# Performance work log

Hardware: AMD Instinct MI355X
Metric: run time of the kernel (lower is better)

The kernel has to match this reference:

```python
import jax, jax.numpy as jnp
import numpy as np

N_PHOTONS = 20_000_000
HEX_R = 24  # axial hex grid radius -> 3R^2+3R+1 = 1801 pixels
SQRT3 = 3.0 ** 0.5


def _build_sensor():
    # Build pointy-top hex pixel centers on an axial grid (replicates hex_centers input),
    # then replicate HexagonalSensor.__init__ lookup-table construction in numpy.
    size = 1.0
    qs, rs = [], []
    for q in range(-HEX_R, HEX_R + 1):
        for r in range(max(-HEX_R, -q - HEX_R), min(HEX_R, -q + HEX_R) + 1):
            qs.append(q); rs.append(r)
    q = np.array(qs, dtype=np.float64); r = np.array(rs, dtype=np.float64)
    centers = np.stack([size * SQRT3 * (q + r / 2.0), size * 1.5 * r], axis=-1)
    n_pixels = centers.shape[0]
    diff = centers[:, None, :] - centers[None, :, :]
    d = np.sqrt((diff ** 2).sum(-1))
    np.fill_diagonal(d, np.inf)
    hex_size = float(d.min() / SQRT3)
    cx, cy = centers[:, 0], centers[:, 1]
    qa = (SQRT3 / 3.0 * cx - cy / 3.0) / hex_size
    ra = (2.0 / 3.0) * cy / hex_size
    q_offset = float(qa[0] - np.round(qa[0]))
    r_offset = float(ra[0] - np.round(ra[0]))
    q_grid = np.round(qa - q_offset).astype(np.int32)
    r_grid = np.round(ra - r_offset).astype(np.int32)
    q_min = int(q_grid.min()); r_min = int(r_grid.min())
    lookup = np.full((int(q_grid.max()) - q_min + 1, int(r_grid.max()) - r_min + 1), -1, dtype=np.int32)
    lookup[q_grid - q_min, r_grid - r_min] = np.arange(n_pixels)
    return hex_size, q_offset, r_offset, q_min, r_min, n_pixels, jnp.asarray(lookup)


def setup_inputs() -> dict:
    key = jax.random.key(0)
    kx, ky, kv = jax.random.split(key, 3)
    hex_size, q_off, r_off, q_min, r_min, n_pixels, lookup = _build_sensor()
    extent = 45.0  # camera footprint (~sqrt(3)*R + margin) so some photons miss (tests masking)
    x = jax.random.uniform(kx, (N_PHOTONS,), minval=-extent, maxval=extent, dtype=jnp.float32)
    y = jax.random.uniform(ky, (N_PHOTONS,), minval=-extent, maxval=extent, dtype=jnp.float32)
    values = jax.random.uniform(kv, (N_PHOTONS,), dtype=jnp.float32)
    return {"x": x, "y": y, "values": values, "lookup_table": lookup,
            "hex_size": hex_size, "q_offset": q_off, "r_offset": r_off,
            "q_min": q_min, "r_min": r_min, "n_pixels": n_pixels}


def _axial_round(q, r):
    s = -q - r
    qr, rr, sr = jnp.round(q), jnp.round(r), jnp.round(s)
    qd, rd, sd = jnp.abs(qr - q), jnp.abs(rr - r), jnp.abs(sr - s)
    qr2 = jnp.where((qd > rd) & (qd > sd), -rr - sr, qr)
    rr2 = jnp.where((rd > qd) & (rd > sd), -qr - sr, rr)
    return qr2, rr2


def reference(x, y, values, lookup_table, hex_size, q_offset, r_offset, q_min, r_min, n_pixels):
    # Cartesian -> axial hex coords
    q = (SQRT3 / 3.0 * x - y / 3.0) / hex_size
    r = (2.0 / 3.0) * y / hex_size
    qg, rg = _axial_round(q - q_offset, r - r_offset)
    q_idx = qg.astype(jnp.int32) - q_min
    r_idx = rg.astype(jnp.int32) - r_min
    Q, R = lookup_table.shape
    in_bounds = (q_idx >= 0) & (q_idx < Q) & (r_idx >= 0) & (r_idx < R)
    pixel_idx = lookup_table[q_idx.clip(0, Q - 1), r_idx.clip(0, R - 1)]
    valid = in_bounds & (pixel_idx >= 0)
    pixel_idx = jnp.where(valid, pixel_idx, 0)
    vals = jnp.where(valid, values, jnp.zeros((), values.dtype))
    return jax.ops.segment_sum(vals, pixel_idx, num_segments=n_pixels)
```

## Files before the change

### kernel.cpp

```cpp
#include <hip/hip_runtime.h>
#include <math.h>


#define FLUSH_P 64

typedef float f32x4 __attribute__((ext_vector_type(4)));

__global__ void hex_zero_kernel(float* __restrict__ p, int n) {
    int i = blockIdx.x * blockDim.x + threadIdx.x;
    if (i < n) p[i] = 0.0f;
}

__global__ __launch_bounds__(256) void hex_reduce_kernel(
    const float* __restrict__ partials, float* __restrict__ out, int n_pixels)
{
    int pix = blockIdx.x * blockDim.x + threadIdx.x;
    if (pix >= n_pixels) return;
    float s = 0.0f;
    #pragma unroll 8
    for (int j = 0; j < FLUSH_P; ++j) s += partials[j * n_pixels + pix];
    out[pix] = s;
}

__global__ __launch_bounds__(256) void hex_bin_kernel(
    const float* __restrict__ x,
    const float* __restrict__ y,
    const float* __restrict__ vals,
    const float* __restrict__ hex_size_p,
    const float* __restrict__ q_off_p,
    const float* __restrict__ r_off_p,
    const int*   __restrict__ q_min_p,
    const int*   __restrict__ r_min_p,
    int Rh,
    int n_pixels, int n_photons,
    float* __restrict__ flush_dst,
    int use_partials)
{
    extern __shared__ float hist[];
    for (int i = threadIdx.x; i < n_pixels; i += blockDim.x) hist[i] = 0.0f;
    __syncthreads();

    const float inv_h = 1.0f / hex_size_p[0];
    const float A  = 0.57735026918962576f * inv_h;
    const float Bn = -(0.33333333333333333f * inv_h);
    const float C  = 0.66666666666666667f * inv_h;
    const float qc = -q_off_p[0];
    const float rc = -r_off_p[0];
    const int   qmin = q_min_p[0];
    const int   rmin = r_min_p[0];

    const unsigned twoR = (unsigned)(2 * Rh);
    const int Rp1 = Rh + 1;

    auto process = [&](float xf, float yf, float vf) {
        float q = fmaf(A, xf, fmaf(Bn, yf, qc));
        float r = fmaf(C, yf, rc);
        float t = q + r;
        float qr = rintf(q);
        float rr = rintf(r);
        float tr = rintf(t);
        float qd = fabsf(qr - q);
        float rd = fabsf(rr - r);
        float td = fabsf(tr - t);
        float q2 = (qd > rd && qd > td) ? (tr - rr) : qr;
        float r2 = (rd > qd && rd > td) ? (tr - qr) : rr;
        int qi = (int)q2 - qmin;
        int ri = (int)r2 - rmin;
        int d  = qi + ri;
        if ((unsigned)qi <= twoR && (unsigned)ri <= twoR &&
            (unsigned)(d - Rh) <= twoR) {
            int u  = max(qi - Rh, 0);
            int p  = qi * Rp1 + ((qi * qi - qi) >> 1) + d - Rh - u * u;
            atomicAdd(&hist[p], vf);
        }
    };

    const int tid    = blockIdx.x * blockDim.x + threadIdx.x;
    const int stride = gridDim.x * blockDim.x;
    const int n8     = n_photons >> 3;

    const f32x4* __restrict__ x4 = (const f32x4*)x;
    const f32x4* __restrict__ y4 = (const f32x4*)y;
    const f32x4* __restrict__ v4 = (const f32x4*)vals;

    f32x4 xa, xb, ya, yb, va, vb;
    int i = tid;
    if (i < n8) {
        int a = 2 * i, b = a + 1;
        xa = __builtin_nontemporal_load(&x4[a]);
        xb = __builtin_nontemporal_load(&x4[b]);
        ya = __builtin_nontemporal_load(&y4[a]);
        yb = __builtin_nontemporal_load(&y4[b]);
        va = __builtin_nontemporal_load(&v4[a]);
        vb = __builtin_nontemporal_load(&v4[b]);
    }
    while (i < n8) {
        int nx = i + stride;
        f32x4 nxa, nxb, nya, nyb, nva, nvb;
        bool has_next = nx < n8;
        if (has_next) {
            int a = 2 * nx, b = a + 1;
            nxa = __builtin_nontemporal_load(&x4[a]);
            nxb = __builtin_nontemporal_load(&x4[b]);
            nya = __builtin_nontemporal_load(&y4[a]);
            nyb = __builtin_nontemporal_load(&y4[b]);
            nva = __builtin_nontemporal_load(&v4[a]);
            nvb = __builtin_nontemporal_load(&v4[b]);
        }
        process(xa.x, ya.x, va.x);
        process(xa.y, ya.y, va.y);
        process(xa.z, ya.z, va.z);
        process(xa.w, ya.w, va.w);
        process(xb.x, yb.x, vb.x);
        process(xb.y, yb.y, vb.y);
        process(xb.z, yb.z, vb.z);
        process(xb.w, yb.w, vb.w);
        if (has_next) {
            xa = nxa; xb = nxb; ya = nya; yb = nyb; va = nva; vb = nvb;
        }
        i = nx;
    }
    for (int t2 = (n8 << 3) + tid; t2 < n_photons; t2 += stride) {
        process(x[t2], y[t2], vals[t2]);
    }

    __syncthreads();
    float* dst = use_partials
        ? flush_dst + (size_t)(blockIdx.x & (FLUSH_P - 1)) * n_pixels
        : flush_dst;
    for (int k = threadIdx.x; k < n_pixels; k += blockDim.x) {
        float h = hist[k];
        if (h != 0.0f) atomicAdd(&dst[k], h);
    }
}

extern "C" void kernel_launch(void* const* d_in, const int* in_sizes, int n_in,
                              void* d_out, int out_size, void* d_ws, size_t ws_size,
                              hipStream_t stream) {
    const float* x      = (const float*)d_in[0];
    const float* y      = (const float*)d_in[1];
    const float* vals   = (const float*)d_in[2];
    const float* hexs   = (const float*)d_in[4];
    const float* qoff   = (const float*)d_in[5];
    const float* roff   = (const float*)d_in[6];
    const int*   qmin   = (const int*)d_in[7];
    const int*   rmin   = (const int*)d_in[8];

    const int n_photons = in_sizes[0];
    const int lut_elems = in_sizes[3];
    const int Q  = (int)(0.5 + sqrt((double)lut_elems));
    const int Rh = (Q - 1) / 2;
    const int n_pixels = out_size;

    float* out = (float*)d_out;
    float* partials = (float*)d_ws;

    const size_t partial_elems = (size_t)FLUSH_P * (size_t)n_pixels;
    const int use_partials = (ws_size >= partial_elems * sizeof(float)) ? 1 : 0;

    const int threads = 256;
    const int blocks  = 2048;
    const size_t lds_bytes = (size_t)n_pixels * sizeof(float);

    if (use_partials) {
        int zn = (int)partial_elems;
        hex_zero_kernel<<<(zn + 255) / 256, 256, 0, stream>>>(partials, zn);
        hex_bin_kernel<<<blocks, threads, lds_bytes, stream>>>(
            x, y, vals, hexs, qoff, roff, qmin, rmin,
            Rh, n_pixels, n_photons, partials, 1);
        hex_reduce_kernel<<<(n_pixels + 255) / 256, 256, 0, stream>>>(
            partials, out, n_pixels);
    } else {
        hex_zero_kernel<<<(n_pixels + 255) / 256, 256, 0, stream>>>(out, n_pixels);
        hex_bin_kernel<<<blocks, threads, lds_bytes, stream>>>(
            x, y, vals, hexs, qoff, roff, qmin, rmin,
            Rh, n_pixels, n_photons, out, 0);
    }
}
```

Before: 79.35 us.

## Deepen load pipeline to five in-flight float4 stages with register rotation

Replaces the double-buffered 8-photon-per-thread loop with a 4-photon-per-iteration loop that keeps five stages of float4 loads in flight, prefetching five strides ahead and rotating through unrolled register slots. Launch bounds now request 4 blocks per CU so the compiler caps register use. The aim is to hide HBM latency in this bandwidth-bound binning pass with more memory-level parallelism per thread. The cost is more live registers, which may force spills under the new occupancy cap, and a changed per-thread access pattern (one float4 per stride instead of two adjacent ones).

```diff
diff --git a/kernel.cpp b/kernel.cpp
--- a/kernel.cpp
+++ b/kernel.cpp
@@ -22,7 +22,7 @@
     out[pix] = s;
 }
 
-__global__ __launch_bounds__(256) void hex_bin_kernel(
+__global__ __launch_bounds__(256, 4) void hex_bin_kernel(
     const float* __restrict__ x,
     const float* __restrict__ y,
     const float* __restrict__ vals,
@@ -77,50 +77,48 @@
 
     const int tid    = blockIdx.x * blockDim.x + threadIdx.x;
     const int stride = gridDim.x * blockDim.x;
-    const int n8     = n_photons >> 3;
+    const int n4     = n_photons >> 2;
 
-    const f32x4* __restrict__ x4 = (const f32x4*)x;
-    const f32x4* __restrict__ y4 = (const f32x4*)y;
-    const f32x4* __restrict__ v4 = (const f32x4*)vals;
+    const f32x4* __restrict__ px = (const f32x4*)x;
+    const f32x4* __restrict__ py = (const f32x4*)y;
+    const f32x4* __restrict__ pv = (const f32x4*)vals;
 
-    f32x4 xa, xb, ya, yb, va, vb;
+    f32x4 x0, y0, v0, x1, y1, v1, x2, y2, v2, x3, y3, v3, x4, y4, v4;
+
+#define LOADS(S, idx) do { int _i = (idx); \
+        x##S = __builtin_nontemporal_load(&px[_i]); \
+        y##S = __builtin_nontemporal_load(&py[_i]); \
+        v##S = __builtin_nontemporal_load(&pv[_i]); } while (0)
+#define PROC(S) do { \
+        process(x##S.x, y##S.x, v##S.x); \
+        process(x##S.y, y##S.y, v##S.y); \
+        process(x##S.z, y##S.z, v##S.z); \
+        process(x##S.w, y##S.w, v##S.w); } while (0)
+#define BODY(S) \
+        if (i >= n4) break; \
+        PROC(S); \
+        { int pf = i + 5 * stride; if (pf < n4) LOADS(S, pf); } \
+        i += stride;
+
+    if (tid + 0 * stride < n4) LOADS(0, tid + 0 * stride);
+    if (tid + 1 * stride < n4) LOADS(1, tid + 1 * stride);
+    if (tid + 2 * stride < n4) LOADS(2, tid + 2 * stride);
+    if (tid + 3 * stride < n4) LOADS(3, tid + 3 * stride);
+    if (tid + 4 * stride < n4) LOADS(4, tid + 4 * stride);
+
     int i = tid;
-    if (i < n8) {
-        int a = 2 * i, b = a + 1;
-        xa = __builtin_nontemporal_load(&x4[a]);
-        xb = __builtin_nontemporal_load(&x4[b]);
-        ya = __builtin_nontemporal_load(&y4[a]);
-        yb = __builtin_nontemporal_load(&y4[b]);
-        va = __builtin_nontemporal_load(&v4[a]);
-        vb = __builtin_nontemporal_load(&v4[b]);
+    for (;;) {
+        BODY(0)
+        BODY(1)
+        BODY(2)
+        BODY(3)
+        BODY(4)
     }
-    while (i < n8) {
-        int nx = i + stride;
-        f32x4 nxa, nxb, nya, nyb, nva, nvb;
-        bool has_next = nx < n8;
-        if (has_next) {
-            int a = 2 * nx, b = a + 1;
-            nxa = __builtin_nontemporal_load(&x4[a]);
-            nxb = __builtin_nontemporal_load(&x4[b]);
-            nya = __builtin_nontemporal_load(&y4[a]);
-            nyb = __builtin_nontemporal_load(&y4[b]);
-            nva = __builtin_nontemporal_load(&v4[a]);
-            nvb = __builtin_nontemporal_load(&v4[b]);
-        }
-        process(xa.x, ya.x, va.x);
-        process(xa.y, ya.y, va.y);
-        process(xa.z, ya.z, va.z);
-        process(xa.w, ya.w, va.w);
-        process(xb.x, yb.x, vb.x);
-        process(xb.y, yb.y, vb.y);
-        process(xb.z, yb.z, vb.z);
-        process(xb.w, yb.w, vb.w);
-        if (has_next) {
-            xa = nxa; xb = nxb; ya = nya; yb = nyb; va = nva; vb = nvb;
-        }
-        i = nx;
-    }
-    for (int t2 = (n8 << 3) + tid; t2 < n_photons; t2 += stride) {
+#undef BODY
+#undef PROC
+#undef LOADS
+
+    for (int t2 = (n4 << 2) + tid; t2 < n_photons; t2 += stride) {
         process(x[t2], y[t2], vals[t2]);
     }
 
```

After: 82.98 us. 1.05x slower.
